# Optimization experiments

Measured on AMD Instinct MI355X. Metric: run time of the kernel, lower is better.

The kernel has to match this reference:

```python
import jax, jax.numpy as jnp
import numpy as np

B, N, DIM = 64, 784, 256
N1, N2, HS, WS, M, D = 1, 4, 28, 7, 8, 2  # x_windows, y_windows, H_sp, W_sp, num_heads, d
HW = HS * WS                              # 196 tokens per window
C = DIM // M                              # 32 channels per head


def setup_inputs() -> dict:
    key = jax.random.key(0)
    ks = jax.random.split(key, 5)
    x = jax.random.normal(ks[0], (B, N, DIM), dtype=jnp.float32)
    Wc = jax.random.normal(ks[1], (DIM, M * D), dtype=jnp.float32) * 0.02
    bc = jax.random.normal(ks[2], (M * D,), dtype=jnp.float32) * 0.02
    Wg = jax.random.normal(ks[3], (HW * D, HW * HW), dtype=jnp.float32) * 0.02
    bg = jax.random.normal(ks[4], (HW * HW,), dtype=jnp.float32) * 0.02
    return {"x": x, "Wc": Wc, "bc": bc, "Wg": Wg, "bg": bg}


def reference(x, Wc, bc, Wg, bg):
    b = x.shape[0]
    # compress: B N C -> B N (m d)
    w = x @ Wc + bc
    # rearrange 'b (n1 h n2 w) (m d) -> b (n1 n2 m) (h w d)'
    w = w.reshape(b, N1, HS, N2, WS, M, D)
    w = w.transpose(0, 1, 3, 5, 2, 4, 6).reshape(b, N1 * N2 * M, HW * D)
    # generate per-window mixing weights: B Nw (HW*HW)
    w = w @ Wg + bg
    w = w.reshape(b, N1 * N2 * M, HW, HW)
    # softmax over dim=-2 (the (h1 w1) source axis)
    w = jax.nn.softmax(w, axis=-2)
    # rearrange x: 'b (n1 h1 n2 w1) (m c) -> b (n1 n2 m) c (h1 w1)'
    xv = x.reshape(b, N1, HS, N2, WS, M, C)
    xv = xv.transpose(0, 1, 3, 5, 6, 2, 4).reshape(b, N1 * N2 * M, C, HW)
    # windowed mixing matmul: (b, Nw, C, HW) @ (b, Nw, HW, HW)
    out = jnp.matmul(xv, w)
    # rearrange back: 'b (n1 n2 m) c (h2 w2) -> b (n1 h2 n2 w2) (m c)'
    out = out.reshape(b, N1, N2, M, C, HS, WS)
    out = out.transpose(0, 1, 5, 2, 6, 3, 4).reshape(b, N1 * HS * N2 * WS, M * C)
    return out
```

## Files before the change

kernel.cpp:

```cpp
#include <hip/hip_runtime.h>
#include <hip/hip_bf16.h>
#include <stdint.h>
#include <stddef.h>

#define NB    64
#define NTOK  784
#define DIMC  256
#define NN2   4
#define NM    8
#define NHW   196
#define NWIN  32
#define NROWS 2048
#define NK    392
#define NKP   448
#define NBIG  38416
#define NIP   200
#define STROW 39200
#define STROW2 39232
#define NPT   39424
#define NTT   307
#define PTS   232

typedef __attribute__((ext_vector_type(4))) float f32x4;
typedef __attribute__((ext_vector_type(8))) short bf16x8;

static __device__ __forceinline__ float bf2f(unsigned short u) {
  union { unsigned int i; float f; } v; v.i = ((unsigned int)u) << 16; return v.f;
}
static __device__ __forceinline__ unsigned short f2bf(float f) {
  union { float f; unsigned int i; } v; v.f = f;
  unsigned int r = v.i + 0x7fffu + ((v.i >> 16) & 1u);
  return (unsigned short)(r >> 16);
}

__global__ __launch_bounds__(256) void k_compress(
    const float* __restrict__ x, const float* __restrict__ Wc,
    const float* __restrict__ bc, unsigned short* __restrict__ Abf) {
  __shared__ float wcs[16 * 256];
  __shared__ float bcs[16];
  const int tid = threadIdx.x;
  const int b  = blockIdx.x / NN2;
  const int n2 = blockIdx.x % NN2;
  for (int idx = tid; idx < 4096; idx += 256) {
    int c = idx >> 4, md = idx & 15;
    wcs[md * 256 + c] = Wc[idx];
  }
  if (tid < 16) bcs[tid] = bc[tid];
  __syncthreads();
  if (tid < NHW) {
    const int h = tid / 7, wcol = tid % 7;
    const int t = h * 28 + n2 * 7 + wcol;
    const float* xp = x + ((size_t)b * NTOK + t) * DIMC;
    float acc[16];
    #pragma unroll
    for (int md = 0; md < 16; ++md) acc[md] = bcs[md];
    for (int c = 0; c < 256; c += 4) {
      const f32x4 xv = *(const f32x4*)(xp + c);
      #pragma unroll
      for (int md = 0; md < 16; ++md) {
        const f32x4 wv = *(const f32x4*)(wcs + md * 256 + c);
        acc[md] += xv[0]*wv[0] + xv[1]*wv[1] + xv[2]*wv[2] + xv[3]*wv[3];
      }
    }
    #pragma unroll
    for (int md = 0; md < 16; ++md) {
      const int m = md >> 1, d = md & 1;
      const int r = b * NWIN + n2 * NM + m;
      Abf[(size_t)r * NKP + tid * 2 + d] = f2bf(acc[md]);
    }
  }
  for (int e = tid; e < NM * (NKP - NK); e += 256) {
    const int m = e / (NKP - NK);
    const int k = NK + (e % (NKP - NK));
    const int r = b * NWIN + n2 * NM + m;
    Abf[(size_t)r * NKP + k] = (k == NK) ? (unsigned short)0x3F80 : 0;
  }
}

__global__ __launch_bounds__(256) void k_wgt(
    const float* __restrict__ Wg, const float* __restrict__ bg,
    unsigned short* __restrict__ Wgbt) {
  __shared__ float tile[64][65];
  const int bid = blockIdx.x;
  const int n0 = (bid % 601) * 64;
  const int k0 = (bid / 601) * 64;
  const int tid = threadIdx.x;
  for (int idx = tid; idx < 4096; idx += 256) {
    const int kk = idx >> 6, nn = idx & 63;
    const int k = k0 + kk, n = n0 + nn;
    float v = 0.f;
    if (n < NBIG) {
      if (k < NK) v = Wg[(size_t)k * NBIG + n];
      else if (k == NK) v = bg[n];
    }
    tile[nn][kk] = v;
  }
  __syncthreads();
  for (int idx = tid; idx < 512; idx += 256) {
    const int nn = idx >> 3, gg = idx & 7;
    const int n = n0 + nn;
    if (n < NBIG) {
      const int i = n / NHW, j = n - (n / NHW) * NHW;
      const int np = j * NIP + i;
      unsigned short u8[8];
      #pragma unroll
      for (int e = 0; e < 8; ++e) u8[e] = f2bf(tile[nn][gg * 8 + e]);
      *(uint4*)&Wgbt[(size_t)np * NKP + k0 + gg * 8] = *(const uint4*)u8;
    }
  }
}

__global__ __launch_bounds__(256) void k_zero(unsigned short* __restrict__ Wgbt) {
  const int bid = blockIdx.x;
  int np;
  if (bid < 784) { const int j = bid >> 2, i = 196 + (bid & 3); np = j * NIP + i; }
  else           { np = STROW + (bid - 784); }
  unsigned int* p = (unsigned int*)(Wgbt + (size_t)np * NKP);
  if (threadIdx.x < 224) p[threadIdx.x] = 0u;
}

__global__ __launch_bounds__(256) void k_gemm(
    const unsigned short* __restrict__ A,
    const unsigned short* __restrict__ Bt,
    unsigned short* __restrict__ E, int mtiles) {
  __shared__ __align__(128) short smem[32768];
  const int tid = threadIdx.x;
  const int w = tid >> 6, lane = tid & 63;
  const int nwg = gridDim.x;
  const int q = nwg >> 3, rr = nwg & 7;
  const int xcd = blockIdx.x & 7, pos = blockIdx.x >> 3;
  const int wg = (xcd < rr ? xcd * (q + 1) : rr * (q + 1) + (xcd - rr) * q) + pos;
  const int nt = wg / mtiles, mt = wg % mtiles;
  const int m0 = mt * 128, n0 = nt * 128;
  const int wm = (w >> 1) * 64, wn = (w & 1) * 64;
  const int lrow = lane >> 3;
  const int lcolsw = ((lane & 7) ^ lrow) * 8;

  const unsigned short* Arow = A  + (size_t)(m0 + w * 32 + lrow) * NKP + lcolsw;
  const unsigned short* Brow = Bt + (size_t)(n0 + w * 32 + lrow) * NKP + lcolsw;

  auto stage = [&](int kt, int buf) {
    #pragma unroll
    for (int is = 0; is < 4; ++is) {
      const int gg = w * 4 + is;
      __builtin_amdgcn_global_load_lds(
          (const __attribute__((address_space(1))) void*)(Arow + (size_t)is * 8 * NKP + kt),
          (__attribute__((address_space(3))) void*)((char*)smem + buf * 16384 + gg * 1024), 16, 0, 0);
      __builtin_amdgcn_global_load_lds(
          (const __attribute__((address_space(1))) void*)(Brow + (size_t)is * 8 * NKP + kt),
          (__attribute__((address_space(3))) void*)((char*)smem + 32768 + buf * 16384 + gg * 1024), 16, 0, 0);
    }
  };

  f32x4 acc[4][4] = {};
  stage(0, 0);
  const int lq = lane >> 4;
  const int lx = (lane & 7);
  #pragma unroll
  for (int t = 0; t < 7; ++t) {
    const int buf = t & 1;
    if (t < 6) {
      stage((t + 1) * 64, buf ^ 1);
      asm volatile("s_waitcnt vmcnt(8)" ::: "memory");
    } else {
      asm volatile("s_waitcnt vmcnt(0)" ::: "memory");
    }
    __builtin_amdgcn_s_barrier();
    __builtin_amdgcn_sched_barrier(0);
    const short* ab = smem + buf * 8192;
    const short* bb = smem + 16384 + buf * 8192;
    #pragma unroll
    for (int kk = 0; kk < 2; ++kk) {
      bf16x8 af[4], bfr[4];
      #pragma unroll
      for (int i = 0; i < 4; ++i) {
        const int row = wm + i * 16 + (lane & 15);
        const int slot = ((kk * 4 + lq) ^ lx) * 8;
        af[i]  = *(const bf16x8*)(ab + row * 64 + slot);
        const int rowb = wn + i * 16 + (lane & 15);
        bfr[i] = *(const bf16x8*)(bb + rowb * 64 + slot);
      }
      #pragma unroll
      for (int mi = 0; mi < 4; ++mi)
        #pragma unroll
        for (int ni = 0; ni < 4; ++ni)
          acc[mi][ni] = __builtin_amdgcn_mfma_f32_16x16x32_bf16(af[mi], bfr[ni], acc[mi][ni], 0, 0, 0);
    }
    __builtin_amdgcn_sched_barrier(0);
    __builtin_amdgcn_s_barrier();
  }

  const int cq = lane >> 4, cr = lane & 15;
  #pragma unroll
  for (int mi = 0; mi < 4; ++mi)
    #pragma unroll
    for (int ni = 0; ni < 4; ++ni)
      #pragma unroll
      for (int e = 0; e < 4; ++e) {
        const int rl = wm + mi * 16 + cq * 4 + e;
        const int cl = wn + ni * 16 + cr;
        smem[rl * 132 + cl] = (short)f2bf(__expf(acc[mi][ni][e]));
      }
  __syncthreads();
  for (int idx = tid; idx < 2048; idx += 256) {
    const int rl = idx >> 4, seg = idx & 15;
    const int col0 = n0 + seg * 8;
    if (col0 < STROW2) {
      const uint4 v = *(const uint4*)&smem[rl * 132 + seg * 8];
      *(uint4*)&E[(size_t)(m0 + rl) * STROW2 + col0] = v;
    }
  }
}

__global__ __launch_bounds__(512) void k_mix(
    const unsigned short* __restrict__ E, const float* __restrict__ x,
    float* __restrict__ out, int row0) {
  __shared__ unsigned short Elds[22528];
  __shared__ unsigned short xvT[32 * PTS];
  const int tid = threadIdx.x, w = tid >> 6, lane = tid & 63;
  const int row = blockIdx.x >> 1, jh = blockIdx.x & 1;
  const int r = row0 + row;
  const int b = r >> 5, win = r & 31, n2 = win >> 3, m = win & 7;

  const unsigned short* Eb = E + (size_t)row * STROW2;
  const int g0 = jh ? 2800 : 0;
  const int nch = jh ? 33 : 44;
  for (int ch = w; ch < nch; ch += 8) {
    const int gr = g0 + ch * 64 + lane;
    if (gr < 4904)
      __builtin_amdgcn_global_load_lds(
          (const __attribute__((address_space(1))) void*)(Eb + (size_t)gr * 8),
          (__attribute__((address_space(3))) void*)((char*)Elds + ch * 1024), 16, 0, 0);
  }

  for (int idx = tid; idx < 1568; idx += 512) {
    const int i = idx >> 3, c4 = (idx & 7) * 4;
    const int t = (i / 7) * 28 + n2 * 7 + (i % 7);
    const f32x4 v = *(const f32x4*)(x + ((size_t)b * NTOK + t) * DIMC + m * 32 + c4);
    xvT[(c4 + 0) * PTS + i] = f2bf(v[0]);
    xvT[(c4 + 1) * PTS + i] = f2bf(v[1]);
    xvT[(c4 + 2) * PTS + i] = f2bf(v[2]);
    xvT[(c4 + 3) * PTS + i] = f2bf(v[3]);
  }
  for (int idx = tid; idx < 32 * (PTS - NHW); idx += 512) {
    const int c = idx / (PTS - NHW), i = NHW + idx % (PTS - NHW);
    xvT[c * PTS + i] = 0;
  }
  __syncthreads();

  bf16x8 bfr[2][7];
  #pragma unroll
  for (int ct = 0; ct < 2; ++ct)
    #pragma unroll
    for (int kk = 0; kk < 7; ++kk)
      bfr[ct][kk] = *(const bf16x8*)&xvT[(ct * 16 + (lane & 15)) * PTS + kk * 32 + (lane >> 4) * 8];
  const bool den = (lane & 15) == 0;
  bf16x8 oneA, oneB;
  #pragma unroll
  for (int e = 0; e < 8; ++e) {
    oneA[e] = den ? (short)0x3F80 : (short)0;
    const int i6 = 192 + (lane >> 4) * 8 + e;
    oneB[e] = (den && i6 < NHW) ? (short)0x3F80 : (short)0;
  }

  const int jt0 = jh ? 7 : 0;
  const int jtend = jh ? 13 : 7;
  for (int jt = jt0 + w; jt < jtend; jt += 8) {
    const int jA = jt * 16 + (lane & 15);
    const int jAc = (jA < NHW) ? jA : NHW - 1;
    const unsigned short* rp = Elds + jAc * NIP - jh * 22400 + (lane >> 4) * 8;
    bf16x8 af[7];
    #pragma unroll
    for (int kk = 0; kk < 7; ++kk) af[kk] = *(const bf16x8*)(rp + kk * 32);
    f32x4 a0 = {0.f,0.f,0.f,0.f}, a1 = {0.f,0.f,0.f,0.f}, ad = {0.f,0.f,0.f,0.f};
    #pragma unroll
    for (int kk = 0; kk < 7; ++kk) {
      a0 = __builtin_amdgcn_mfma_f32_16x16x32_bf16(af[kk], bfr[0][kk], a0, 0, 0, 0);
      a1 = __builtin_amdgcn_mfma_f32_16x16x32_bf16(af[kk], bfr[1][kk], a1, 0, 0, 0);
      ad = __builtin_amdgcn_mfma_f32_16x16x32_bf16(af[kk], (kk < 6) ? oneA : oneB, ad, 0, 0, 0);
    }
    const int c = lane & 15;
    #pragma unroll
    for (int e = 0; e < 4; ++e) {
      const int j = jt * 16 + (lane >> 4) * 4 + e;
      const float dv = __shfl(ad[e], lane & 48);
      if (j < NHW) {
        const float inv = 1.f / dv;
        const int t2 = (j / 7) * 28 + n2 * 7 + (j % 7);
        float* op = out + ((size_t)b * NTOK + t2) * DIMC + m * 32;
        op[c] = a0[e] * inv;
        op[c + 16] = a1[e] * inv;
      }
    }
  }
}

extern "C" void kernel_launch(void* const* d_in, const int* in_sizes, int n_in,
                              void* d_out, int out_size, void* d_ws, size_t ws_size,
                              hipStream_t stream) {
  const float* x  = (const float*)d_in[0];
  const float* Wc = (const float*)d_in[1];
  const float* bc = (const float*)d_in[2];
  const float* Wg = (const float*)d_in[3];
  const float* bg = (const float*)d_in[4];
  float* out = (float*)d_out;

  char* ws = (char*)d_ws;
  const size_t wgbt_bytes = (size_t)NPT * NKP * 2;
  const size_t a_bytes    = (size_t)NROWS * NKP * 2;
  unsigned short* Wgbt = (unsigned short*)ws;
  unsigned short* Abf  = (unsigned short*)(ws + wgbt_bytes);
  unsigned short* E    = (unsigned short*)(ws + wgbt_bytes + a_bytes);
  const size_t fixed = wgbt_bytes + a_bytes;
  const size_t srow_bytes = (size_t)STROW2 * 2;

  size_t avail = (ws_size > fixed) ? (ws_size - fixed) : 0;
  int rows_chunk = (int)(avail / srow_bytes);
  rows_chunk = (rows_chunk / 128) * 128;
  if (rows_chunk > NROWS) rows_chunk = NROWS;
  if (rows_chunk < 128)  rows_chunk = 128;

  hipLaunchKernelGGL(k_compress, dim3(NB * NN2), dim3(256), 0, stream, x, Wc, bc, Abf);
  hipLaunchKernelGGL(k_wgt, dim3(601 * 7), dim3(256), 0, stream, Wg, bg, Wgbt);
  hipLaunchKernelGGL(k_zero, dim3(1008), dim3(256), 0, stream, Wgbt);
  for (int row0 = 0; row0 < NROWS; row0 += rows_chunk) {
    int rc = NROWS - row0; if (rc > rows_chunk) rc = rows_chunk;
    hipLaunchKernelGGL(k_gemm, dim3((rc / 128) * NTT), dim3(256), 0, stream,
                       Abf + (size_t)row0 * NKP, Wgbt, E, rc / 128);
    hipLaunchKernelGGL(k_mix, dim3(rc * 2), dim3(512), 0, stream, E, x, out, row0);
  }
}
```

Baseline: 213.2 us.

## Pre-swizzle A into MFMA fragment layout and load it directly to registers

Adds a k_afrag kernel that rewrites the compressed A matrix into per-lane MFMA fragment order. The GEMM then loads A fragments straight from global memory into double-buffered registers instead of staging them through LDS. This halves LDS use and traffic per tile, which may allow more waves per CU, and removes the A LDS reads. In exchange it adds a kernel launch, extra register pressure, and direct global loads whose latency must be covered by the prefetch.

```diff
diff --git a/kernel.cpp b/kernel.cpp
--- a/kernel.cpp
+++ b/kernel.cpp
@@ -13,6 +13,7 @@
 #define NROWS 2048
 #define NK    392
 #define NKP   448
+#define KKF   14
 #define NBIG  38416
 #define NIP   200
 #define STROW 39200
@@ -74,6 +75,16 @@
     const int k = NK + (e % (NKP - NK));
     const int r = b * NWIN + n2 * NM + m;
     Abf[(size_t)r * NKP + k] = (k == NK) ? (unsigned short)0x3F80 : 0;
+  }
+}
+
+__global__ __launch_bounds__(256) void k_afrag(
+    const unsigned short* __restrict__ A, unsigned short* __restrict__ Af) {
+  const int mf = blockIdx.x;
+  for (int idx = threadIdx.x; idx < KKF * 64; idx += 256) {
+    const int kk = idx >> 6, l = idx & 63;
+    const bf16x8 v = *(const bf16x8*)(A + (size_t)(mf * 16 + (l & 15)) * NKP + kk * 32 + (l >> 4) * 8);
+    *(bf16x8*)(Af + ((size_t)(mf * KKF + kk) * 64 + l) * 8) = v;
   }
 }
 
@@ -120,10 +131,10 @@
 }
 
 __global__ __launch_bounds__(256) void k_gemm(
-    const unsigned short* __restrict__ A,
+    const unsigned short* __restrict__ Af,
     const unsigned short* __restrict__ Bt,
-    unsigned short* __restrict__ E, int mtiles) {
-  __shared__ __align__(128) short smem[32768];
+    unsigned short* __restrict__ E, int row0, int mtiles) {
+  __shared__ __align__(128) short smem[17408];
   const int tid = threadIdx.x;
   const int w = tid >> 6, lane = tid & 63;
   const int nwg = gridDim.x;
@@ -136,55 +147,61 @@
   const int lrow = lane >> 3;
   const int lcolsw = ((lane & 7) ^ lrow) * 8;
 
-  const unsigned short* Arow = A  + (size_t)(m0 + w * 32 + lrow) * NKP + lcolsw;
   const unsigned short* Brow = Bt + (size_t)(n0 + w * 32 + lrow) * NKP + lcolsw;
+  const unsigned short* aptr = Af + (size_t)((row0 + m0 + wm) >> 4) * (KKF * 512) + lane * 8;
 
   auto stage = [&](int kt, int buf) {
     #pragma unroll
     for (int is = 0; is < 4; ++is) {
       const int gg = w * 4 + is;
       __builtin_amdgcn_global_load_lds(
-          (const __attribute__((address_space(1))) void*)(Arow + (size_t)is * 8 * NKP + kt),
+          (const __attribute__((address_space(1))) void*)(Brow + (size_t)is * 8 * NKP + kt),
           (__attribute__((address_space(3))) void*)((char*)smem + buf * 16384 + gg * 1024), 16, 0, 0);
-      __builtin_amdgcn_global_load_lds(
-          (const __attribute__((address_space(1))) void*)(Brow + (size_t)is * 8 * NKP + kt),
-          (__attribute__((address_space(3))) void*)((char*)smem + 32768 + buf * 16384 + gg * 1024), 16, 0, 0);
     }
   };
 
+  bf16x8 ar[2][2][4];
   f32x4 acc[4][4] = {};
+  #pragma unroll
+  for (int kk2 = 0; kk2 < 2; ++kk2)
+    #pragma unroll
+    for (int i = 0; i < 4; ++i)
+      ar[0][kk2][i] = *(const bf16x8*)(aptr + ((size_t)i * KKF + kk2) * 512);
   stage(0, 0);
+
   const int lq = lane >> 4;
   const int lx = (lane & 7);
   #pragma unroll
   for (int t = 0; t < 7; ++t) {
     const int buf = t & 1;
     if (t < 6) {
+      #pragma unroll
+      for (int kk2 = 0; kk2 < 2; ++kk2)
+        #pragma unroll
+        for (int i = 0; i < 4; ++i)
+          ar[buf ^ 1][kk2][i] = *(const bf16x8*)(aptr + ((size_t)i * KKF + 2 * (t + 1) + kk2) * 512);
       stage((t + 1) * 64, buf ^ 1);
-      asm volatile("s_waitcnt vmcnt(8)" ::: "memory");
+      asm volatile("s_waitcnt vmcnt(12)" ::: "memory");
     } else {
       asm volatile("s_waitcnt vmcnt(0)" ::: "memory");
     }
     __builtin_amdgcn_s_barrier();
     __builtin_amdgcn_sched_barrier(0);
-    const short* ab = smem + buf * 8192;
-    const short* bb = smem + 16384 + buf * 8192;
+    const short* bb = smem + buf * 8192;
     #pragma unroll
     for (int kk = 0; kk < 2; ++kk) {
-      bf16x8 af[4], bfr[4];
+      bf16x8 bfr[4];
       #pragma unroll
       for (int i = 0; i < 4; ++i) {
-        const int row = wm + i * 16 + (lane & 15);
+        const int rowb = wn + i * 16 + (lane & 15);
         const int slot = ((kk * 4 + lq) ^ lx) * 8;
-        af[i]  = *(const bf16x8*)(ab + row * 64 + slot);
-        const int rowb = wn + i * 16 + (lane & 15);
         bfr[i] = *(const bf16x8*)(bb + rowb * 64 + slot);
       }
       #pragma unroll
       for (int mi = 0; mi < 4; ++mi)
         #pragma unroll
         for (int ni = 0; ni < 4; ++ni)
-          acc[mi][ni] = __builtin_amdgcn_mfma_f32_16x16x32_bf16(af[mi], bfr[ni], acc[mi][ni], 0, 0, 0);
+          acc[mi][ni] = __builtin_amdgcn_mfma_f32_16x16x32_bf16(ar[buf][kk][mi], bfr[ni], acc[mi][ni], 0, 0, 0);
     }
     __builtin_amdgcn_sched_barrier(0);
     __builtin_amdgcn_s_barrier();
@@ -308,10 +325,12 @@
   char* ws = (char*)d_ws;
   const size_t wgbt_bytes = (size_t)NPT * NKP * 2;
   const size_t a_bytes    = (size_t)NROWS * NKP * 2;
+  const size_t af_bytes   = (size_t)128 * KKF * 512 * 2;
   unsigned short* Wgbt = (unsigned short*)ws;
   unsigned short* Abf  = (unsigned short*)(ws + wgbt_bytes);
-  unsigned short* E    = (unsigned short*)(ws + wgbt_bytes + a_bytes);
-  const size_t fixed = wgbt_bytes + a_bytes;
+  unsigned short* Af   = (unsigned short*)(ws + wgbt_bytes + a_bytes);
+  unsigned short* E    = (unsigned short*)(ws + wgbt_bytes + a_bytes + af_bytes);
+  const size_t fixed = wgbt_bytes + a_bytes + af_bytes;
   const size_t srow_bytes = (size_t)STROW2 * 2;
 
   size_t avail = (ws_size > fixed) ? (ws_size - fixed) : 0;
@@ -321,12 +340,13 @@
   if (rows_chunk < 128)  rows_chunk = 128;
 
   hipLaunchKernelGGL(k_compress, dim3(NB * NN2), dim3(256), 0, stream, x, Wc, bc, Abf);
+  hipLaunchKernelGGL(k_afrag, dim3(NROWS / 16), dim3(256), 0, stream, Abf, Af);
   hipLaunchKernelGGL(k_wgt, dim3(601 * 7), dim3(256), 0, stream, Wg, bg, Wgbt);
   hipLaunchKernelGGL(k_zero, dim3(1008), dim3(256), 0, stream, Wgbt);
   for (int row0 = 0; row0 < NROWS; row0 += rows_chunk) {
     int rc = NROWS - row0; if (rc > rows_chunk) rc = rows_chunk;
     hipLaunchKernelGGL(k_gemm, dim3((rc / 128) * NTT), dim3(256), 0, stream,
-                       Abf + (size_t)row0 * NKP, Wgbt, E, rc / 128);
+                       Af, Wgbt, E, row0, rc / 128);
     hipLaunchKernelGGL(k_mix, dim3(rc * 2), dim3(512), 0, stream, E, x, out, row0);
   }
 }
```

New measurement: 222.1 us. 1.04x slower.
